# Optimization experiments

Measured on AMD Instinct MI355X. Metric: run time of the kernel, lower is better.

## Reference

```python
import jax, jax.numpy as jnp
import numpy as np

B, T, D, N = 4, 1024, 1024, 16
H = D // N
SCALE = H ** -0.5
NEG_INF = float('-inf')


def setup_inputs() -> dict:
    key = jax.random.key(0)
    ks = jax.random.split(key, 6)
    x = jax.random.normal(ks[0], (B, T, D), dtype=jnp.float32)
    key_padding_mask = jax.random.uniform(ks[1], (B, T)) < 0.1  # True = padded key
    # xavier-ish scaling for weights
    proj_weight = jax.random.normal(ks[2], (3 * D, D), dtype=jnp.float32) * (2.0 / (4 * D)) ** 0.5
    proj_bias = jnp.zeros((3 * D,), dtype=jnp.float32)
    sign_w = jax.random.normal(ks[3], (2 * D, D), dtype=jnp.float32) * (2.0 / (3 * D)) ** 0.5
    sign_b = jnp.zeros((2 * D,), dtype=jnp.float32)
    out_w = jax.random.normal(ks[4], (D, D), dtype=jnp.float32) * (1.0 / D) ** 0.5
    out_b = jnp.zeros((D,), dtype=jnp.float32)
    return {"x": x, "key_padding_mask": key_padding_mask,
            "proj_weight": proj_weight, "proj_bias": proj_bias,
            "sign_w": sign_w, "sign_b": sign_b,
            "out_w": out_w, "out_b": out_b}


def _heads(t):
    # [B, S, D] -> [B, N, S, H]
    return t.reshape(t.shape[0], t.shape[1], N, H).transpose(0, 2, 1, 3)


def reference(x, key_padding_mask, proj_weight, proj_bias, sign_w, sign_b, out_w, out_b):
    # self-attention path: fused in-projection, chunk order is (k, v, q)
    kvq = x @ proj_weight.T + proj_bias            # [B, T, 3D]
    k, v, q = jnp.split(kvq, 3, axis=-1)
    # sign projections (sign_q and sign_k both enabled): chunk into (sq, sk)
    sqk = x @ sign_w.T + sign_b                    # [B, T, 2D]
    sq, sk = jnp.split(sqk, 2, axis=-1)

    q, k, v = _heads(q), _heads(k), _heads(v)      # [B, N, T, H]
    sq = jax.nn.relu(_heads(sq))                   # q_activation = relu
    sk = jax.nn.relu(_heads(sk))                   # k_activation = relu

    attn_weight = jnp.einsum('bnth,bnsh->bnts', q, k) * SCALE   # [B, N, T, T]
    sign_weight = jnp.tanh(jnp.einsum('bnth,bnsh->bnts', sq, sk))

    kp = key_padding_mask[:, None, None, :]        # [B, 1, 1, T]
    attn_weight = jnp.where(kp, NEG_INF, attn_weight)
    sign_weight = jnp.where(attn_weight == NEG_INF, 0.0, sign_weight)

    ctx = jnp.einsum('bnts,bnsh->bnth', sign_weight, v)         # [B, N, T, H]
    ctx = ctx.transpose(0, 2, 1, 3).reshape(x.shape[0], x.shape[1], D)
    out = ctx @ out_w.T + out_b
    return out, sign_weight
```

## Files before the change

kernel.cpp:

```cpp
#include <hip/hip_runtime.h>

#define B_ 4
#define T_ 1024
#define D_ 1024
#define N_ 16
#define H_ 64

typedef __attribute__((ext_vector_type(8))) short bf16x8;
typedef __attribute__((ext_vector_type(4))) float f32x4;

static __device__ __forceinline__ unsigned short f2bf(float f) {
  unsigned u = __float_as_uint(f);
  u += 0x7fff + ((u >> 16) & 1);
  return (unsigned short)(u >> 16);
}

static __device__ __forceinline__ unsigned pk2(float a, float b) {
  return (unsigned)f2bf(a) | ((unsigned)f2bf(b) << 16);
}

static __device__ __forceinline__ float fast_tanh(float x) {
  float e = __expf(2.0f * x);
  return 1.0f - 2.0f / (e + 1.0f);
}

__global__ __launch_bounds__(256) void prep_kernel(
    const float* __restrict__ x, const float* __restrict__ sign_w,
    const float* __restrict__ proj_w_v, const float* __restrict__ out_w,
    const unsigned char* __restrict__ raw,
    unsigned short* __restrict__ xb, unsigned short* __restrict__ swb,
    unsigned short* __restrict__ pwb, unsigned short* __restrict__ owb,
    unsigned long long* __restrict__ mask64) {
  if (blockIdx.x == 0) {
    __shared__ int s_flag;
    if (threadIdx.x == 0) s_flag = 0;
    __syncthreads();
    int any = 0;
    for (int i = threadIdx.x; i < 4096; i += 256)
      if (i & 3) any |= (int)raw[i];
    if (any) atomicOr(&s_flag, 1);
    __syncthreads();
    int byte_mode = s_flag;
    const int* iraw = (const int*)raw;
    int w = threadIdx.x >> 6, l = threadIdx.x & 63;
    for (int k = 0; k < 16; ++k) {
      int pair = w * 16 + k;
      int idx = pair * 64 + l;
      int v = byte_mode ? (int)raw[idx] : iraw[idx];
      unsigned long long bal = __ballot(v != 0);
      if (l == 0) mask64[pair] = bal;
    }
  }
  const int n0 = 1048576, n1 = 524288, n2 = 262144;
  const int total = n0 + n1 + n2 + 262144;
  for (int i = blockIdx.x * 256 + threadIdx.x; i < total;
       i += gridDim.x * 256) {
    const float* src;
    unsigned short* dst;
    int off;
    if (i < n0) { src = x; dst = xb; off = i; }
    else if (i < n0 + n1) { src = sign_w; dst = swb; off = i - n0; }
    else if (i < n0 + n1 + n2) { src = proj_w_v; dst = pwb; off = i - n0 - n1; }
    else { src = out_w; dst = owb; off = i - n0 - n1 - n2; }
    float4 v = ((const float4*)src)[off];
    uint2 pk;
    pk.x = pk2(v.x, v.y);
    pk.y = pk2(v.z, v.w);
    ((uint2*)dst)[off] = pk;
  }
}

template <int MF, int NF>
static __device__ __forceinline__ void gemm_core(
    const unsigned short* __restrict__ A, const unsigned short* __restrict__ W,
    const float* __restrict__ bias, void* __restrict__ Cv,
    int N, int K, int relu, int out_mode, size_t bm, size_t bn,
    unsigned short* As, unsigned short* Ws, int tid) {
  int l = tid & 63, w = tid >> 6;
  int l15 = l & 15, l4 = l >> 4;
  int wr = w >> 1, wc = w & 1;

  f32x4 acc[MF][NF];
#pragma unroll
  for (int m = 0; m < MF; ++m)
#pragma unroll
    for (int n = 0; n < NF; ++n) acc[m][n] = (f32x4){0.f, 0.f, 0.f, 0.f};

  for (int k0 = 0; k0 < K; k0 += 64) {
    __syncthreads();
#pragma unroll
    for (int i = 0; i < MF; ++i) {
      int seg = i * 256 + tid;
      int row = seg >> 3, cb = (seg & 7) << 4;
      __builtin_amdgcn_global_load_lds(
          (const __attribute__((address_space(1))) void*)
              ((const char*)(A + (bm + row) * K + k0) + cb),
          (__attribute__((address_space(3))) void*)(As + (size_t)(i * 256 + w * 64) * 8),
          16, 0, 0);
    }
#pragma unroll
    for (int i = 0; i < NF; ++i) {
      int seg = i * 256 + tid;
      int row = seg >> 3, cb = (seg & 7) << 4;
      __builtin_amdgcn_global_load_lds(
          (const __attribute__((address_space(1))) void*)
              ((const char*)(W + (bn + row) * K + k0) + cb),
          (__attribute__((address_space(3))) void*)(Ws + (size_t)(i * 256 + w * 64) * 8),
          16, 0, 0);
    }
    __syncthreads();

#pragma unroll
    for (int ks = 0; ks < 2; ++ks) {
      bf16x8 af[MF], bf[NF];
#pragma unroll
      for (int m = 0; m < MF; ++m)
        af[m] = *(const bf16x8*)(As + (wr * (MF * 16) + m * 16 + l15) * 64 +
                                 ks * 32 + l4 * 8);
#pragma unroll
      for (int n = 0; n < NF; ++n)
        bf[n] = *(const bf16x8*)(Ws + (wc * (NF * 16) + n * 16 + l15) * 64 +
                                 ks * 32 + l4 * 8);
#pragma unroll
      for (int m = 0; m < MF; ++m)
#pragma unroll
        for (int n = 0; n < NF; ++n)
          acc[m][n] = __builtin_amdgcn_mfma_f32_16x16x32_bf16(
              af[m], bf[n], acc[m][n], 0, 0, 0);
    }
  }

#pragma unroll
  for (int n = 0; n < NF; ++n) {
    size_t c = bn + wc * (NF * 16) + n * 16 + l15;
    float bv = bias[c];
#pragma unroll
    for (int m = 0; m < MF; ++m) {
      float o[4];
#pragma unroll
      for (int rr = 0; rr < 4; ++rr) {
        o[rr] = acc[m][n][rr] + bv;
        if (relu) o[rr] = fmaxf(o[rr], 0.0f);
      }
      size_t r0 = bm + wr * (MF * 16) + m * 16 + l4 * 4;
      if (out_mode == 0) {
        float* C = (float*)Cv;
#pragma unroll
        for (int rr = 0; rr < 4; ++rr) C[(r0 + rr) * N + c] = o[rr];
      } else if (out_mode == 1) {
        unsigned short* Cb = (unsigned short*)Cv;
#pragma unroll
        for (int rr = 0; rr < 4; ++rr) Cb[(r0 + rr) * N + c] = f2bf(o[rr]);
      } else {
        unsigned short* Cb = (unsigned short*)Cv;
        size_t bbase = (bm >> 10) << 10;
        int tloc = (int)(bm & 1023) + wr * (MF * 16) + m * 16 + l4 * 4;
        uint2 pk;
        pk.x = pk2(o[0], o[1]);
        pk.y = pk2(o[2], o[3]);
        *(uint2*)(Cb + (bbase + c) * 1024 + tloc) = pk;
      }
    }
  }
}

__global__ __launch_bounds__(256, 3) void gemm_qv_kernel(
    const unsigned short* __restrict__ xb, const unsigned short* __restrict__ swb,
    const unsigned short* __restrict__ pwb, const float* __restrict__ sign_b,
    const float* __restrict__ proj_b_v, unsigned short* __restrict__ sqkb,
    unsigned short* __restrict__ vtb) {
  __shared__ __align__(16) unsigned short As[128 * 64];
  __shared__ __align__(16) unsigned short Ws[128 * 64];
  size_t bm = (size_t)blockIdx.x * 128;
  int by = blockIdx.y;
  if (by < 16)
    gemm_core<4, 4>(xb, swb, sign_b, sqkb, 2048, 1024, 1, 1,
                    bm, (size_t)by * 128, As, Ws, threadIdx.x);
  else
    gemm_core<4, 4>(xb, pwb, proj_b_v, vtb, 1024, 1024, 0, 2,
                    bm, (size_t)(by - 16) * 128, As, Ws, threadIdx.x);
}

__global__ __launch_bounds__(256, 3) void gemm_out_kernel(
    const unsigned short* __restrict__ ctxb, const unsigned short* __restrict__ owb,
    const float* __restrict__ out_b, float* __restrict__ out) {
  __shared__ __align__(16) unsigned short As[64 * 64];
  __shared__ __align__(16) unsigned short Ws[128 * 64];
  gemm_core<2, 4>(ctxb, owb, out_b, out, 1024, 1024, 0, 0,
                  (size_t)blockIdx.x * 64, (size_t)blockIdx.y * 128,
                  As, Ws, threadIdx.x);
}

__global__ __launch_bounds__(256, 4) void attn_mfma_kernel(
    const unsigned short* __restrict__ sqkb,
    const unsigned short* __restrict__ vtb,
    const unsigned long long* __restrict__ mask64,
    float* __restrict__ sign_out,
    unsigned short* __restrict__ ctx) {
  __shared__ __align__(16) char sk_lds[2][64 * 128];
  __shared__ __align__(16) char vt_lds[2][64 * 128];
  __shared__ __align__(16) char p_lds[4 * 16 * 128];

  int bid = (blockIdx.x & 7) * 128 + (blockIdx.x >> 3);
  int tt = bid & 15;
  int bn = bid >> 4;
  int n = bn & 15, b = bn >> 4;
  int t0 = tt * 64;
  int tid = threadIdx.x;
  int l = tid & 63, w = tid >> 6;
  int l15 = l & 15, l4 = l >> 4;
  int trow_g = t0 + w * 16 + l15;

  bf16x8 aq[2];
#pragma unroll
  for (int ks = 0; ks < 2; ++ks)
    aq[ks] = *(const bf16x8*)(sqkb + (size_t)(b * 1024 + trow_g) * 2048 +
                              n * 64 + ks * 32 + l4 * 8);

  f32x4 cacc[4];
#pragma unroll
  for (int ht = 0; ht < 4; ++ht) cacc[ht] = (f32x4){0.f, 0.f, 0.f, 0.f};

  const char* sk_base = (const char*)(sqkb) + 2048 + (size_t)n * 128;
  const char* vt_base = (const char*)(vtb) + (size_t)bn * 64 * 2048;

  char* pw = p_lds + w * 2048;

#pragma unroll
  for (int i = 0; i < 2; ++i) {
    int seg = i * 256 + tid;
    int row = seg >> 3, cb = (seg & 7) << 4;
    int sc = cb ^ ((row & 7) << 4);
    __builtin_amdgcn_global_load_lds(
        (const __attribute__((address_space(1))) void*)
            (sk_base + (size_t)(b * 1024 + row) * 4096 + sc),
        (__attribute__((address_space(3))) void*)(sk_lds[0] + (i * 256 + w * 64) * 16),
        16, 0, 0);
    __builtin_amdgcn_global_load_lds(
        (const __attribute__((address_space(1))) void*)
            (vt_base + (size_t)row * 2048 + sc),
        (__attribute__((address_space(3))) void*)(vt_lds[0] + (i * 256 + w * 64) * 16),
        16, 0, 0);
  }

  int cur = 0;
  for (int ci = 0; ci < 16; ++ci) {
    int s0 = ci * 64;
    __syncthreads();

    if (ci < 15) {
      int s1 = s0 + 64;
#pragma unroll
      for (int i = 0; i < 2; ++i) {
        int seg = i * 256 + tid;
        int row = seg >> 3, cb = (seg & 7) << 4;
        int sc = cb ^ ((row & 7) << 4);
        __builtin_amdgcn_global_load_lds(
            (const __attribute__((address_space(1))) void*)
                (sk_base + (size_t)(b * 1024 + s1 + row) * 4096 + sc),
            (__attribute__((address_space(3))) void*)(sk_lds[cur ^ 1] + (i * 256 + w * 64) * 16),
            16, 0, 0);
        __builtin_amdgcn_global_load_lds(
            (const __attribute__((address_space(1))) void*)
                (vt_base + (size_t)row * 2048 + (size_t)s1 * 2 + sc),
            (__attribute__((address_space(3))) void*)(vt_lds[cur ^ 1] + (i * 256 + w * 64) * 16),
            16, 0, 0);
      }
    }

    unsigned long long mbits = mask64[b * 16 + ci];
    const char* skc = sk_lds[cur];
    const char* vtc = vt_lds[cur];

#pragma unroll
    for (int st = 0; st < 4; ++st) {
      f32x4 pc = (f32x4){0.f, 0.f, 0.f, 0.f};
      __builtin_amdgcn_s_setprio(1);
#pragma unroll
      for (int ks = 0; ks < 2; ++ks) {
        int srow = st * 16 + l15;
        bf16x8 ak = *(const bf16x8*)(skc + srow * 128 +
            ((ks * 64 + l4 * 16) ^ ((srow & 7) << 4)));
        pc = __builtin_amdgcn_mfma_f32_16x16x32_bf16(ak, aq[ks], pc, 0, 0, 0);
      }
      __builtin_amdgcn_s_setprio(0);
      f32x4 o;
#pragma unroll
      for (int rr = 0; rr < 4; ++rr) {
        int s_idx = st * 16 + l4 * 4 + rr;
        int msk = (int)((mbits >> s_idx) & 1ULL);
        o[rr] = msk ? 0.0f : fast_tanh(pc[rr]);
      }
      uint2 pk;
      pk.x = pk2(o[0], o[1]);
      pk.y = pk2(o[2], o[3]);
      *(uint2*)(pw + l15 * 128 + ((st * 32 + l4 * 8) ^ ((l15 & 7) << 4))) = pk;
    }

#pragma unroll
    for (int p = 0; p < 4; ++p) {
      int row = p * 4 + (l >> 4);
      uint2 pk = *(const uint2*)(pw + row * 128 +
                                 (((l & 15) * 8) ^ ((row & 7) << 4)));
      f32x4 o;
      o[0] = __uint_as_float(pk.x << 16);
      o[1] = __uint_as_float(pk.x & 0xffff0000u);
      o[2] = __uint_as_float(pk.y << 16);
      o[3] = __uint_as_float(pk.y & 0xffff0000u);
      __builtin_nontemporal_store(o,
          (f32x4*)(sign_out + ((size_t)bn * 1024 + t0 + w * 16 + row) * 1024 +
                   s0 + (l & 15) * 4));
    }

    __builtin_amdgcn_s_setprio(1);
#pragma unroll
    for (int ks = 0; ks < 2; ++ks) {
      bf16x8 bp = *(const bf16x8*)(pw + l15 * 128 +
          ((ks * 64 + l4 * 16) ^ ((l15 & 7) << 4)));
#pragma unroll
      for (int ht = 0; ht < 4; ++ht) {
        int hrow = ht * 16 + l15;
        bf16x8 av = *(const bf16x8*)(vtc + hrow * 128 +
            ((ks * 64 + l4 * 16) ^ ((hrow & 7) << 4)));
        cacc[ht] = __builtin_amdgcn_mfma_f32_16x16x32_bf16(
            av, bp, cacc[ht], 0, 0, 0);
      }
    }
    __builtin_amdgcn_s_setprio(0);
    cur ^= 1;
  }

#pragma unroll
  for (int ht = 0; ht < 4; ++ht) {
    uint2 pk;
    pk.x = pk2(cacc[ht][0], cacc[ht][1]);
    pk.y = pk2(cacc[ht][2], cacc[ht][3]);
    *(uint2*)(ctx + ((size_t)(b * 1024 + trow_g)) * 1024 + n * 64 + ht * 16 +
              l4 * 4) = pk;
  }
}

extern "C" void kernel_launch(void* const* d_in, const int* in_sizes, int n_in,
                              void* d_out, int out_size, void* d_ws, size_t ws_size,
                              hipStream_t stream) {
  const float* x = (const float*)d_in[0];
  const unsigned char* kp = (const unsigned char*)d_in[1];
  const float* proj_w = (const float*)d_in[2];
  const float* proj_b = (const float*)d_in[3];
  const float* sign_w = (const float*)d_in[4];
  const float* sign_b = (const float*)d_in[5];
  const float* out_w = (const float*)d_in[6];
  const float* out_b = (const float*)d_in[7];

  float* out = (float*)d_out;
  float* sign_out = out + (size_t)B_ * T_ * D_;

  char* ws = (char*)d_ws;
  unsigned short* xb   = (unsigned short*)ws;
  unsigned short* swb  = (unsigned short*)(ws + ((size_t)8 << 20));
  unsigned short* pwb  = (unsigned short*)(ws + ((size_t)12 << 20));
  unsigned short* owb  = (unsigned short*)(ws + ((size_t)14 << 20));
  unsigned short* sqkb = (unsigned short*)(ws + ((size_t)16 << 20));
  unsigned short* vtb  = (unsigned short*)(ws + ((size_t)32 << 20));
  unsigned long long* mask64 = (unsigned long long*)(ws + ((size_t)40 << 20));
  unsigned short* ctxb = xb;

  const int M = B_ * T_;

  prep_kernel<<<2048, 256, 0, stream>>>(x, sign_w, proj_w + (size_t)D_ * D_,
                                        out_w, kp, xb, swb, pwb, owb, mask64);

  {
    dim3 g(M / 128, 24);
    gemm_qv_kernel<<<g, 256, 0, stream>>>(xb, swb, pwb, sign_b, proj_b + D_,
                                          sqkb, vtb);
  }
  attn_mfma_kernel<<<B_ * N_ * (T_ / 64), 256, 0, stream>>>(sqkb, vtb, mask64,
                                                            sign_out, ctxb);
  {
    dim3 g(M / 64, 1024 / 128);
    gemm_out_kernel<<<g, 256, 0, stream>>>(ctxb, owb, out_b, out);
  }
}
```

Measured before the change: 150.4 us.

## Double attention query tile per block to reuse staged K/V tiles

Each attention block now covers 128 query rows instead of 64, so every wave computes two 16-row MFMA tiles against the same staged sk and vT LDS tiles. This halves the number of blocks and the repeated global-to-LDS loads of K and V per query, amortizing staging traffic across more MFMA work. In exchange, register and LDS use per block grow (launch bounds drop from 4 to 3), and the grid shrinks to 512 blocks, which may underfill the GPU. The kernel is likely dominated by the large fp32 sign_weight store, so it is unclear how much the reduced load traffic helps.

```diff
diff --git a/kernel.cpp b/kernel.cpp
--- a/kernel.cpp
+++ b/kernel.cpp
@@ -191,7 +191,7 @@
                   As, Ws, threadIdx.x);
 }
 
-__global__ __launch_bounds__(256, 4) void attn_mfma_kernel(
+__global__ __launch_bounds__(256, 3) void attn_mfma_kernel(
     const unsigned short* __restrict__ sqkb,
     const unsigned short* __restrict__ vtb,
     const unsigned long long* __restrict__ mask64,
@@ -199,32 +199,36 @@
     unsigned short* __restrict__ ctx) {
   __shared__ __align__(16) char sk_lds[2][64 * 128];
   __shared__ __align__(16) char vt_lds[2][64 * 128];
-  __shared__ __align__(16) char p_lds[4 * 16 * 128];
-
-  int bid = (blockIdx.x & 7) * 128 + (blockIdx.x >> 3);
-  int tt = bid & 15;
-  int bn = bid >> 4;
+  __shared__ __align__(16) char p_lds[4 * 32 * 128];
+
+  int bid = (blockIdx.x & 7) * 64 + (blockIdx.x >> 3);
+  int tt = bid & 7;
+  int bn = bid >> 3;
   int n = bn & 15, b = bn >> 4;
-  int t0 = tt * 64;
+  int t0 = tt * 128;
   int tid = threadIdx.x;
   int l = tid & 63, w = tid >> 6;
   int l15 = l & 15, l4 = l >> 4;
-  int trow_g = t0 + w * 16 + l15;
-
-  bf16x8 aq[2];
-#pragma unroll
-  for (int ks = 0; ks < 2; ++ks)
-    aq[ks] = *(const bf16x8*)(sqkb + (size_t)(b * 1024 + trow_g) * 2048 +
-                              n * 64 + ks * 32 + l4 * 8);
-
-  f32x4 cacc[4];
-#pragma unroll
-  for (int ht = 0; ht < 4; ++ht) cacc[ht] = (f32x4){0.f, 0.f, 0.f, 0.f};
+
+  bf16x8 aq[2][2];
+#pragma unroll
+  for (int mt = 0; mt < 2; ++mt)
+#pragma unroll
+    for (int ks = 0; ks < 2; ++ks)
+      aq[mt][ks] = *(const bf16x8*)(sqkb +
+          (size_t)(b * 1024 + t0 + w * 32 + mt * 16 + l15) * 2048 +
+          n * 64 + ks * 32 + l4 * 8);
+
+  f32x4 cacc[4][2];
+#pragma unroll
+  for (int ht = 0; ht < 4; ++ht)
+#pragma unroll
+    for (int mt = 0; mt < 2; ++mt) cacc[ht][mt] = (f32x4){0.f, 0.f, 0.f, 0.f};
 
   const char* sk_base = (const char*)(sqkb) + 2048 + (size_t)n * 128;
   const char* vt_base = (const char*)(vtb) + (size_t)bn * 64 * 2048;
 
-  char* pw = p_lds + w * 2048;
+  char* pw = p_lds + w * 4096;
 
 #pragma unroll
   for (int i = 0; i < 2; ++i) {
@@ -274,31 +278,41 @@
 
 #pragma unroll
     for (int st = 0; st < 4; ++st) {
-      f32x4 pc = (f32x4){0.f, 0.f, 0.f, 0.f};
+      f32x4 pc[2];
+      pc[0] = (f32x4){0.f, 0.f, 0.f, 0.f};
+      pc[1] = (f32x4){0.f, 0.f, 0.f, 0.f};
       __builtin_amdgcn_s_setprio(1);
 #pragma unroll
       for (int ks = 0; ks < 2; ++ks) {
         int srow = st * 16 + l15;
         bf16x8 ak = *(const bf16x8*)(skc + srow * 128 +
             ((ks * 64 + l4 * 16) ^ ((srow & 7) << 4)));
-        pc = __builtin_amdgcn_mfma_f32_16x16x32_bf16(ak, aq[ks], pc, 0, 0, 0);
+#pragma unroll
+        for (int mt = 0; mt < 2; ++mt)
+          pc[mt] = __builtin_amdgcn_mfma_f32_16x16x32_bf16(
+              ak, aq[mt][ks], pc[mt], 0, 0, 0);
       }
       __builtin_amdgcn_s_setprio(0);
-      f32x4 o;
-#pragma unroll
-      for (int rr = 0; rr < 4; ++rr) {
-        int s_idx = st * 16 + l4 * 4 + rr;
-        int msk = (int)((mbits >> s_idx) & 1ULL);
-        o[rr] = msk ? 0.0f : fast_tanh(pc[rr]);
-      }
-      uint2 pk;
-      pk.x = pk2(o[0], o[1]);
-      pk.y = pk2(o[2], o[3]);
-      *(uint2*)(pw + l15 * 128 + ((st * 32 + l4 * 8) ^ ((l15 & 7) << 4))) = pk;
-    }
-
-#pragma unroll
-    for (int p = 0; p < 4; ++p) {
+#pragma unroll
+      for (int mt = 0; mt < 2; ++mt) {
+        f32x4 o;
+#pragma unroll
+        for (int rr = 0; rr < 4; ++rr) {
+          int s_idx = st * 16 + l4 * 4 + rr;
+          int msk = (int)((mbits >> s_idx) & 1ULL);
+          o[rr] = msk ? 0.0f : fast_tanh(pc[mt][rr]);
+        }
+        uint2 pk;
+        pk.x = pk2(o[0], o[1]);
+        pk.y = pk2(o[2], o[3]);
+        int trow = mt * 16 + l15;
+        *(uint2*)(pw + trow * 128 +
+                  ((st * 32 + l4 * 8) ^ ((trow & 7) << 4))) = pk;
+      }
+    }
+
+#pragma unroll
+    for (int p = 0; p < 8; ++p) {
       int row = p * 4 + (l >> 4);
       uint2 pk = *(const uint2*)(pw + row * 128 +
                                  (((l & 15) * 8) ^ ((row & 7) << 4)));
@@ -308,22 +322,29 @@
       o[2] = __uint_as_float(pk.y << 16);
       o[3] = __uint_as_float(pk.y & 0xffff0000u);
       __builtin_nontemporal_store(o,
-          (f32x4*)(sign_out + ((size_t)bn * 1024 + t0 + w * 16 + row) * 1024 +
+          (f32x4*)(sign_out + ((size_t)bn * 1024 + t0 + w * 32 + row) * 1024 +
                    s0 + (l & 15) * 4));
     }
 
     __builtin_amdgcn_s_setprio(1);
 #pragma unroll
     for (int ks = 0; ks < 2; ++ks) {
-      bf16x8 bp = *(const bf16x8*)(pw + l15 * 128 +
-          ((ks * 64 + l4 * 16) ^ ((l15 & 7) << 4)));
+      bf16x8 bp[2];
+#pragma unroll
+      for (int mt = 0; mt < 2; ++mt) {
+        int trow = mt * 16 + l15;
+        bp[mt] = *(const bf16x8*)(pw + trow * 128 +
+            ((ks * 64 + l4 * 16) ^ ((trow & 7) << 4)));
+      }
 #pragma unroll
       for (int ht = 0; ht < 4; ++ht) {
         int hrow = ht * 16 + l15;
         bf16x8 av = *(const bf16x8*)(vtc + hrow * 128 +
             ((ks * 64 + l4 * 16) ^ ((hrow & 7) << 4)));
-        cacc[ht] = __builtin_amdgcn_mfma_f32_16x16x32_bf16(
-            av, bp, cacc[ht], 0, 0, 0);
+#pragma unroll
+        for (int mt = 0; mt < 2; ++mt)
+          cacc[ht][mt] = __builtin_amdgcn_mfma_f32_16x16x32_bf16(
+              av, bp[mt], cacc[ht][mt], 0, 0, 0);
       }
     }
     __builtin_amdgcn_s_setprio(0);
@@ -331,13 +352,16 @@
   }
 
 #pragma unroll
-  for (int ht = 0; ht < 4; ++ht) {
-    uint2 pk;
-    pk.x = pk2(cacc[ht][0], cacc[ht][1]);
-    pk.y = pk2(cacc[ht][2], cacc[ht][3]);
-    *(uint2*)(ctx + ((size_t)(b * 1024 + trow_g)) * 1024 + n * 64 + ht * 16 +
-              l4 * 4) = pk;
-  }
+  for (int ht = 0; ht < 4; ++ht)
+#pragma unroll
+    for (int mt = 0; mt < 2; ++mt) {
+      int t = t0 + w * 32 + mt * 16 + l15;
+      uint2 pk;
+      pk.x = pk2(cacc[ht][mt][0], cacc[ht][mt][1]);
+      pk.y = pk2(cacc[ht][mt][2], cacc[ht][mt][3]);
+      *(uint2*)(ctx + ((size_t)(b * 1024 + t)) * 1024 + n * 64 + ht * 16 +
+                l4 * 4) = pk;
+    }
 }
 
 extern "C" void kernel_launch(void* const* d_in, const int* in_sizes, int n_in,
@@ -375,8 +399,8 @@
     gemm_qv_kernel<<<g, 256, 0, stream>>>(xb, swb, pwb, sign_b, proj_b + D_,
                                           sqkb, vtb);
   }
-  attn_mfma_kernel<<<B_ * N_ * (T_ / 64), 256, 0, stream>>>(sqkb, vtb, mask64,
-                                                            sign_out, ctxb);
+  attn_mfma_kernel<<<B_ * N_ * (T_ / 128), 256, 0, stream>>>(sqkb, vtb, mask64,
+                                                             sign_out, ctxb);
   {
     dim3 g(M / 64, 1024 / 128);
     gemm_out_kernel<<<g, 256, 0, stream>>>(ctxb, owb, out_b, out);
```

Measured after the change: 151.2 us. Within noise of the previous version (+0.5%).
